# Performance work log

Measured on AMD Instinct MI355X. Metric: run time of the kernel, lower is better.

The kernel has to match this reference:

```python
import jax, jax.numpy as jnp
import numpy as np
import math

NUM_HEADS = 16
SEGMENT_SIZE = 128
DILATION = 2


def hilbert_map(seq_len: int) -> np.ndarray:
    """Boustrophedon ('Hilbert') permutation, matching the torch reference."""
    if seq_len <= 64:
        return np.arange(seq_len, dtype=np.int64)
    g = int(math.ceil(math.sqrt(seq_len)))
    fm = np.zeros(seq_len, dtype=np.int64)
    idx = 0
    for row in range(g):
        cols = range(g) if row % 2 == 0 else range(g - 1, -1, -1)
        for col in cols:
            lp = row * g + col
            if lp < seq_len and idx < seq_len:
                fm[lp] = idx
                idx += 1
    return fm


def setup_inputs() -> dict:
    key = jax.random.key(0)
    k1, k2, k3 = jax.random.split(key, 3)
    B, S, D = 2, 8192, 1024
    x = jax.random.normal(k1, (B, S, D), dtype=jnp.float32)
    W_qkv = jax.random.normal(k2, (D, 3 * D), dtype=jnp.float32) * 0.02
    W_out = jax.random.normal(k3, (D, D), dtype=jnp.float32) * 0.02
    return {"x": x, "W_qkv": W_qkv, "W_out": W_out}


def reference(x, W_qkv, W_out):
    B, S, Dm = x.shape
    H, Dh = NUM_HEADS, Dm // NUM_HEADS
    seg, dil = SEGMENT_SIZE, DILATION
    scale = Dh ** -0.5

    qkv = (x @ W_qkv).reshape(B, S, 3, H, Dh)
    q = jnp.transpose(qkv[:, :, 0], (0, 2, 1, 3))  # [B,H,S,Dh]
    k = jnp.transpose(qkv[:, :, 1], (0, 2, 1, 3))
    v = jnp.transpose(qkv[:, :, 2], (0, 2, 1, 3))

    # Hilbert reorder (active since S > 64)
    m = jnp.asarray(hilbert_map(S))
    q, k, v = q[:, :, m], k[:, :, m], v[:, :, m]

    # Vectorized segment-local dilated attention (S % seg == 0 here)
    nseg = S // seg
    qs = q.reshape(B, H, nseg, seg, Dh)
    ks = k.reshape(B, H, nseg, seg, Dh)[:, :, :, ::dil]  # dilated keys
    vs = v.reshape(B, H, nseg, seg, Dh)[:, :, :, ::dil]
    scores = jnp.einsum('bhnqd,bhnkd->bhnqk', qs, ks) * scale
    attn = jax.nn.softmax(scores, axis=-1)
    out = jnp.einsum('bhnqk,bhnkd->bhnqd', attn, vs).reshape(B, H, S, Dh)

    # Reverse Hilbert ordering
    inv = jnp.argsort(m)
    out = out[:, :, inv]

    out = jnp.transpose(out, (0, 2, 1, 3)).reshape(B, S, Dm)
    return out @ W_out
```

## Files before the change

kernel.cpp:

```cpp
#include <hip/hip_runtime.h>
#include <stdint.h>

typedef unsigned short ushort_t;
typedef __bf16 bf16x8 __attribute__((ext_vector_type(8)));
typedef float  f32x4  __attribute__((ext_vector_type(4)));
typedef float  f32x16 __attribute__((ext_vector_type(16)));

#define DEV static __device__ __forceinline__

DEV ushort_t f2bf(float f){
  union { float f; unsigned u; } x; x.f = f;
  unsigned u = x.u;
  return (ushort_t)((u + 0x7fffu + ((u >> 16) & 1u)) >> 16);
}

DEV int hmap(int p){
  int r = p / 91;
  int c = p - r * 91;
  return (r & 1) ? (r * 91 + 90 - c) : p;
}

DEV void async16(const void* g, void* l){
  __builtin_amdgcn_global_load_lds(
      (const __attribute__((address_space(1))) unsigned*)g,
      (__attribute__((address_space(3))) unsigned*)l, 16, 0, 0);
}

template<int GATHER>
DEV int arow_map(int r){
  if (GATHER == 0) return r;
  if (GATHER == 1){ int b = r >> 13, p = r & 8191; return b * 8192 + hmap(p); }
  int b = r >> 12, rem = r & 4095, seg = rem >> 6, j = rem & 63;
  return b * 8192 + hmap(seg * 128 + 2 * j);
}

__global__ void cast_kernel(const float* __restrict__ in, ushort_t* __restrict__ out, int n4){
  int i = blockIdx.x * blockDim.x + threadIdx.x;
  if (i < n4){
    float4 v = ((const float4*)in)[i];
    ushort4 o;
    o.x = f2bf(v.x); o.y = f2bf(v.y); o.z = f2bf(v.z); o.w = f2bf(v.w);
    ((ushort4*)out)[i] = o;
  }
}

__global__ void transpose_cast(const float* __restrict__ W, ushort_t* __restrict__ WT,
                               int rows, int cols){
  __shared__ ushort_t t[64 * 66];
  int tid = threadIdx.x;
  int c0 = blockIdx.x * 64, r0 = blockIdx.y * 64;
  int cl = tid & 63, rb = tid >> 6;
  for (int i = 0; i < 16; ++i){
    int r = rb + i * 4;
    t[r * 66 + cl] = f2bf(W[(size_t)(r0 + r) * cols + c0 + cl]);
  }
  __syncthreads();
  int rr = tid & 63, cb = tid >> 6;
  for (int i = 0; i < 16; ++i){
    int cc = cb + i * 4;
    WT[(size_t)(c0 + cc) * rows + r0 + rr] = t[rr * 66 + cc];
  }
}

template<int OUT_BF16, int GATHER>
__global__ __launch_bounds__(256, 2) void gemm_bt(const ushort_t* __restrict__ A,
                                                  const ushort_t* __restrict__ BT,
                                                  void* __restrict__ Cout,
                                                  int M, int N, int K){
  __shared__ ushort_t As[128 * 64];
  __shared__ ushort_t Bs[256 * 64];
  int tid  = threadIdx.x;
  int lane = tid & 63, w = tid >> 6;
  int l31 = lane & 31, lh = lane >> 5;

  int mtc = M >> 7;
  int o  = blockIdx.x;
  int nt = o / mtc, mt = o - nt * mtc;
  int m0 = mt * 128, n0 = nt * 256;

  int wm = (w >> 1) * 64, wn = (w & 1) * 128;

  f32x16 acc[2][4];
  #pragma unroll
  for (int a = 0; a < 8; ++a)
    #pragma unroll
    for (int b = 0; b < 16; ++b) acc[a >> 2][a & 3][b] = 0.f;

  int rbase = tid >> 3, slot = tid & 7;
  int g0 = (slot ^ (rbase & 7)) * 8;
  size_t asrc[4];
  #pragma unroll
  for (int i = 0; i < 4; ++i)
    asrc[i] = (size_t)arow_map<GATHER>(m0 + rbase + 32 * i) * K + g0;
  size_t bsrc0 = (size_t)(n0 + rbase) * K + g0;

  int aoff[2][4], boff[4][4];
  #pragma unroll
  for (int mi = 0; mi < 2; ++mi){
    int r = wm + mi * 32 + l31;
    #pragma unroll
    for (int kc = 0; kc < 4; ++kc)
      aoff[mi][kc] = r * 64 + ((kc * 2 + lh) ^ (r & 7)) * 8;
  }
  #pragma unroll
  for (int ni = 0; ni < 4; ++ni){
    int r = wn + ni * 32 + l31;
    #pragma unroll
    for (int kc = 0; kc < 4; ++kc)
      boff[ni][kc] = r * 64 + ((kc * 2 + lh) ^ (r & 7)) * 8;
  }

  for (int k0 = 0; k0 < K; k0 += 64){
    __syncthreads();
    #pragma unroll
    for (int i = 0; i < 4; ++i)
      async16(&A[asrc[i] + k0], &As[(size_t)(256 * i + tid) * 8]);
    #pragma unroll
    for (int i = 0; i < 8; ++i)
      async16(&BT[bsrc0 + (size_t)(32 * i) * K + k0], &Bs[(size_t)(256 * i + tid) * 8]);
    __syncthreads();

    #pragma unroll
    for (int kc = 0; kc < 4; ++kc){
      bf16x8 af[2], bg[4];
      af[0] = *(const bf16x8*)&As[aoff[0][kc]];
      af[1] = *(const bf16x8*)&As[aoff[1][kc]];
      #pragma unroll
      for (int ni = 0; ni < 4; ++ni)
        bg[ni] = *(const bf16x8*)&Bs[boff[ni][kc]];
      #pragma unroll
      for (int mi = 0; mi < 2; ++mi)
        #pragma unroll
        for (int ni = 0; ni < 4; ++ni)
          acc[mi][ni] = __builtin_amdgcn_mfma_f32_32x32x16_bf16(af[mi], bg[ni], acc[mi][ni], 0, 0, 0);
    }
  }

  #pragma unroll
  for (int mi = 0; mi < 2; ++mi){
    #pragma unroll
    for (int ni = 0; ni < 4; ++ni){
      f32x16 v = acc[mi][ni];
      #pragma unroll
      for (int reg = 0; reg < 16; ++reg){
        int r = m0 + wm + mi * 32 + (reg & 3) + 8 * (reg >> 2) + 4 * lh;
        size_t idx = (size_t)r * N + n0 + wn + ni * 32 + l31;
        if (OUT_BF16) ((ushort_t*)Cout)[idx] = f2bf(v[reg]);
        else          ((float*)   Cout)[idx] = v[reg];
      }
    }
  }
}

__global__ __launch_bounds__(256) void attn_kernel(const ushort_t* __restrict__ Qb,
                                                   const ushort_t* __restrict__ KV,
                                                   ushort_t* __restrict__ aout){
  __shared__ ushort_t Qs[128 * 72];
  __shared__ ushort_t Ks[64 * 72];
  __shared__ ushort_t Vt[64 * 72];
  int tid  = threadIdx.x;
  int lane = tid & 63, w = tid >> 6;
  int qd = lane >> 4, md = lane & 15;
  int seg = blockIdx.x, h = blockIdx.y, b = blockIdx.z;
  int p0 = seg * 128;

  for (int it = 0; it < 4; ++it){
    int q = it * 256 + tid;
    int r = q >> 3, ch = q & 7;
    uint4 d = *(const uint4*)&Qb[(size_t)(b * 8192 + p0 + r) * 1024 + h * 64 + ch * 8];
    *(uint4*)&Qs[r * 72 + ch * 8] = d;
  }
  for (int it = 0; it < 2; ++it){
    int q = it * 256 + tid;
    int r = q >> 3, ch = q & 7;
    uint4 d = *(const uint4*)&KV[(size_t)(b * 4096 + seg * 64 + r) * 2048 + h * 64 + ch * 8];
    *(uint4*)&Ks[r * 72 + ch * 8] = d;
  }
  for (int it = 0; it < 2; ++it){
    int q = it * 256 + tid;
    int r = q >> 3, ch = q & 7;
    union { uint4 v; ushort_t u[8]; } d;
    d.v = *(const uint4*)&KV[(size_t)(b * 4096 + seg * 64 + r) * 2048 + 1024 + h * 64 + ch * 8];
    for (int e = 0; e < 8; ++e) Vt[(ch * 8 + e) * 72 + r] = d.u[e];
  }
  __syncthreads();

  f32x4 z = {0.f, 0.f, 0.f, 0.f};
  f32x4 sc[2][4];
  for (int mi = 0; mi < 2; ++mi) for (int ni = 0; ni < 4; ++ni) sc[mi][ni] = z;
  for (int kc = 0; kc < 2; ++kc){
    bf16x8 aq[2], bk[4];
    for (int mi = 0; mi < 2; ++mi)
      aq[mi] = *(const bf16x8*)&Qs[(w * 32 + mi * 16 + md) * 72 + kc * 32 + qd * 8];
    for (int ni = 0; ni < 4; ++ni)
      bk[ni] = *(const bf16x8*)&Ks[(ni * 16 + md) * 72 + kc * 32 + qd * 8];
    for (int mi = 0; mi < 2; ++mi)
      for (int ni = 0; ni < 4; ++ni)
        sc[mi][ni] = __builtin_amdgcn_mfma_f32_16x16x32_bf16(aq[mi], bk[ni], sc[mi][ni], 0, 0, 0);
  }

  const float scale = 0.125f;
  ushort_t* Ps = Qs;
  for (int mi = 0; mi < 2; ++mi){
    for (int i = 0; i < 4; ++i){
      float mx = sc[mi][0][i];
      for (int ni = 1; ni < 4; ++ni) mx = fmaxf(mx, sc[mi][ni][i]);
      for (int d = 1; d < 16; d <<= 1) mx = fmaxf(mx, __shfl_xor(mx, d));
      float e[4], sum = 0.f;
      for (int ni = 0; ni < 4; ++ni){ e[ni] = __expf((sc[mi][ni][i] - mx) * scale); sum += e[ni]; }
      for (int d = 1; d < 16; d <<= 1) sum += __shfl_xor(sum, d);
      float inv = 1.0f / sum;
      int r = w * 32 + mi * 16 + qd * 4 + i;
      for (int ni = 0; ni < 4; ++ni)
        Ps[r * 72 + ni * 16 + md] = f2bf(e[ni] * inv);
    }
  }

  f32x4 oc[2][4];
  for (int mi = 0; mi < 2; ++mi) for (int ni = 0; ni < 4; ++ni) oc[mi][ni] = z;
  for (int kc = 0; kc < 2; ++kc){
    bf16x8 ap[2], bv[4];
    for (int mi = 0; mi < 2; ++mi)
      ap[mi] = *(const bf16x8*)&Ps[(w * 32 + mi * 16 + md) * 72 + kc * 32 + qd * 8];
    for (int ni = 0; ni < 4; ++ni)
      bv[ni] = *(const bf16x8*)&Vt[(ni * 16 + md) * 72 + kc * 32 + qd * 8];
    for (int mi = 0; mi < 2; ++mi)
      for (int ni = 0; ni < 4; ++ni)
        oc[mi][ni] = __builtin_amdgcn_mfma_f32_16x16x32_bf16(ap[mi], bv[ni], oc[mi][ni], 0, 0, 0);
  }

  for (int mi = 0; mi < 2; ++mi){
    for (int i = 0; i < 4; ++i){
      int rl = w * 32 + mi * 16 + qd * 4 + i;
      for (int ni = 0; ni < 4; ++ni)
        Ps[rl * 72 + ni * 16 + md] = f2bf(oc[mi][ni][i]);
    }
  }
  __syncthreads();
  for (int it = 0; it < 4; ++it){
    int q = it * 256 + tid;
    int r = q >> 3, ch = q & 7;
    int s = hmap(p0 + r);
    *(uint4*)&aout[(size_t)(b * 8192 + s) * 1024 + h * 64 + ch * 8] =
        *(const uint4*)&Qs[r * 72 + ch * 8];
  }
}

extern "C" void kernel_launch(void* const* d_in, const int* in_sizes, int n_in,
                              void* d_out, int out_size, void* d_ws, size_t ws_size,
                              hipStream_t stream){
  const float* x    = (const float*)d_in[0];
  const float* Wqkv = (const float*)d_in[1];
  const float* Wout = (const float*)d_in[2];
  float* out = (float*)d_out;

  char* ws = (char*)d_ws;
  ushort_t* xb    = (ushort_t*)(ws);
  ushort_t* WqT   = (ushort_t*)(ws + 33554432);
  ushort_t* WoT   = (ushort_t*)(ws + 39845888);
  ushort_t* Qbuf  = (ushort_t*)(ws + 41943040);
  ushort_t* KVbuf = (ushort_t*)(ws + 75497472);
  ushort_t* aoutb = (ushort_t*)(ws + 109051904);

  cast_kernel<<<16384, 256, 0, stream>>>(x, xb, (16384 * 1024) / 4);
  transpose_cast<<<dim3(48, 16), 256, 0, stream>>>(Wqkv, WqT, 1024, 3072);
  transpose_cast<<<dim3(16, 16), 256, 0, stream>>>(Wout, WoT, 1024, 1024);
  gemm_bt<1, 1><<<4 * 128, 256, 0, stream>>>(xb, WqT, Qbuf, 16384, 1024, 1024);
  gemm_bt<1, 2><<<8 * 64, 256, 0, stream>>>(xb, WqT + (size_t)1024 * 1024, KVbuf, 8192, 2048, 1024);
  attn_kernel<<<dim3(64, 16, 2), 256, 0, stream>>>(Qbuf, KVbuf, aoutb);
  gemm_bt<0, 0><<<4 * 128, 256, 0, stream>>>(aoutb, WoT, out, 16384, 1024, 1024);
}
```

Before: 274.0 us.

## Rewrite GEMM as 256x256 tile, 512-thread, double-buffered async pipeline with XCD swizzle

After: 273.2 us. No clear change (-0.3%).

```diff
diff --git a/kernel.cpp b/kernel.cpp
--- a/kernel.cpp
+++ b/kernel.cpp
@@ -4,7 +4,6 @@
 typedef unsigned short ushort_t;
 typedef __bf16 bf16x8 __attribute__((ext_vector_type(8)));
 typedef float  f32x4  __attribute__((ext_vector_type(4)));
-typedef float  f32x16 __attribute__((ext_vector_type(16)));
 
 #define DEV static __device__ __forceinline__
 
@@ -62,91 +61,124 @@
   }
 }
 
+
+#define BARRIER() asm volatile("s_barrier" ::: "memory")
+#define LGKM0()   asm volatile("s_waitcnt lgkmcnt(0)" ::: "memory")
+#define VMCNT4()  asm volatile("s_waitcnt vmcnt(4)" ::: "memory")
+#define VMCNT0()  asm volatile("s_waitcnt vmcnt(0)" ::: "memory")
+
+#define STAGE_A(T1, HT)                                                        \
+  if ((T1) < NT){                                                              \
+    ushort_t* d_ = &smem[((((T1) & 1)) << 15) + ((HT) << 13) + tid * 8];       \
+    async16(&A[asrc[HT][0] + (size_t)(T1) * 64], d_);                          \
+    async16(&A[asrc[HT][1] + (size_t)(T1) * 64], d_ + 4096);                   \
+  }
+
+#define STAGE_B(T2, HT)                                                        \
+  if ((T2) < NT){                                                              \
+    ushort_t* d_ = &smem[((((T2) & 1)) << 15) + 16384 + ((HT) << 13) + tid * 8];\
+    async16(&BT[bsrc[HT][0] + (size_t)(T2) * 64], d_);                         \
+    async16(&BT[bsrc[HT][1] + (size_t)(T2) * 64], d_ + 4096);                  \
+  }
+
+#define PHASE(MI0, STAGE_STMT, PRE_BAR2)                                       \
+  {                                                                            \
+    bf16x8 af[2][2];                                                           \
+    _Pragma("unroll") for (int m2 = 0; m2 < 2; ++m2)                           \
+      _Pragma("unroll") for (int kk = 0; kk < 2; ++kk)                         \
+        af[m2][kk] = *(const bf16x8*)&Ab[((MI0) + m2) * 1024 + axor[kk]];      \
+    STAGE_STMT;                                                                \
+    BARRIER();                                                                 \
+    LGKM0();                                                                   \
+    __builtin_amdgcn_s_setprio(1);                                             \
+    _Pragma("unroll") for (int kk = 0; kk < 2; ++kk)                           \
+      _Pragma("unroll") for (int ni = 0; ni < 4; ++ni)                         \
+        _Pragma("unroll") for (int m2 = 0; m2 < 2; ++m2)                       \
+          acc[(MI0) + m2][ni] = __builtin_amdgcn_mfma_f32_16x16x32_bf16(       \
+              af[m2][kk], bv[ni][kk], acc[(MI0) + m2][ni], 0, 0, 0);           \
+    __builtin_amdgcn_s_setprio(0);                                             \
+    PRE_BAR2;                                                                  \
+    BARRIER();                                                                 \
+  }
+
 template<int OUT_BF16, int GATHER>
-__global__ __launch_bounds__(256, 2) void gemm_bt(const ushort_t* __restrict__ A,
+__global__ __launch_bounds__(512, 2) void gemm_bt(const ushort_t* __restrict__ A,
                                                   const ushort_t* __restrict__ BT,
                                                   void* __restrict__ Cout,
                                                   int M, int N, int K){
-  __shared__ ushort_t As[128 * 64];
-  __shared__ ushort_t Bs[256 * 64];
-  int tid  = threadIdx.x;
+  __shared__ __align__(16) ushort_t smem[65536];
+  const int NT = K >> 6;
+  int tid = threadIdx.x;
   int lane = tid & 63, w = tid >> 6;
-  int l31 = lane & 31, lh = lane >> 5;
-
-  int mtc = M >> 7;
-  int o  = blockIdx.x;
-  int nt = o / mtc, mt = o - nt * mtc;
-  int m0 = mt * 128, n0 = nt * 256;
-
-  int wm = (w >> 1) * 64, wn = (w & 1) * 128;
-
-  f32x16 acc[2][4];
+  int md = lane & 15, qd = lane >> 4;
+  int wm = w >> 2, wn = w & 3;
+
+  int nwg = gridDim.x;
+  int orig = blockIdx.x;
+  int wg = (orig & 7) * (nwg >> 3) + (orig >> 3);
+  int mtc = M >> 8;
+  int mt = wg % mtc, nt = wg / mtc;
+  int m0 = mt << 8, n0 = nt << 8;
+
+  int rbase = tid >> 3;
+  int g0 = ((tid & 7) ^ (rbase & 7)) * 8;
+  size_t asrc[2][2], bsrc[2][2];
+  #pragma unroll
+  for (int ht = 0; ht < 2; ++ht)
+    #pragma unroll
+    for (int i = 0; i < 2; ++i){
+      asrc[ht][i] = (size_t)arow_map<GATHER>(m0 + ht * 128 + i * 64 + rbase) * K + g0;
+      bsrc[ht][i] = (size_t)(n0 + ht * 128 + i * 64 + rbase) * K + g0;
+    }
+
+  int abase0 = (wm * 128 + md) * 64;
+  int bbase0 = 16384 + (wn * 64 + md) * 64;
+  int axor[2] = { (qd ^ (md & 7)) * 8, ((4 + qd) ^ (md & 7)) * 8 };
+
+  f32x4 acc[8][4];
   #pragma unroll
   for (int a = 0; a < 8; ++a)
     #pragma unroll
-    for (int b = 0; b < 16; ++b) acc[a >> 2][a & 3][b] = 0.f;
-
-  int rbase = tid >> 3, slot = tid & 7;
-  int g0 = (slot ^ (rbase & 7)) * 8;
-  size_t asrc[4];
+    for (int b = 0; b < 4; ++b)
+      #pragma unroll
+      for (int e = 0; e < 4; ++e) acc[a][b][e] = 0.f;
+
+  STAGE_B(0, 0); STAGE_B(0, 1);
+  STAGE_A(0, 0); STAGE_A(0, 1);
+  STAGE_B(1, 0); STAGE_B(1, 1);
+  VMCNT4();
+  BARRIER();
+
+  for (int t = 0; t < NT; ++t){
+    const ushort_t* Ab = &smem[((t & 1) << 15) + abase0];
+    const ushort_t* Bb = &smem[((t & 1) << 15) + bbase0];
+
+    bf16x8 bv[4][2];
+    #pragma unroll
+    for (int ni = 0; ni < 4; ++ni)
+      #pragma unroll
+      for (int kk = 0; kk < 2; ++kk)
+        bv[ni][kk] = *(const bf16x8*)&Bb[ni * 1024 + axor[kk]];
+
+    PHASE(0, STAGE_A(t + 1, 0), ((void)0));
+    PHASE(2, STAGE_A(t + 1, 1), ((void)0));
+    PHASE(4, STAGE_B(t + 2, 0), ((void)0));
+    PHASE(6, STAGE_B(t + 2, 1),
+          if (t < NT - 2) VMCNT4(); else VMCNT0());
+  }
+
+  int crow0 = m0 + wm * 128 + qd * 4;
+  int ccol0 = n0 + wn * 64 + md;
   #pragma unroll
-  for (int i = 0; i < 4; ++i)
-    asrc[i] = (size_t)arow_map<GATHER>(m0 + rbase + 32 * i) * K + g0;
-  size_t bsrc0 = (size_t)(n0 + rbase) * K + g0;
-
-  int aoff[2][4], boff[4][4];
-  #pragma unroll
-  for (int mi = 0; mi < 2; ++mi){
-    int r = wm + mi * 32 + l31;
-    #pragma unroll
-    for (int kc = 0; kc < 4; ++kc)
-      aoff[mi][kc] = r * 64 + ((kc * 2 + lh) ^ (r & 7)) * 8;
-  }
-  #pragma unroll
-  for (int ni = 0; ni < 4; ++ni){
-    int r = wn + ni * 32 + l31;
-    #pragma unroll
-    for (int kc = 0; kc < 4; ++kc)
-      boff[ni][kc] = r * 64 + ((kc * 2 + lh) ^ (r & 7)) * 8;
-  }
-
-  for (int k0 = 0; k0 < K; k0 += 64){
-    __syncthreads();
-    #pragma unroll
-    for (int i = 0; i < 4; ++i)
-      async16(&A[asrc[i] + k0], &As[(size_t)(256 * i + tid) * 8]);
-    #pragma unroll
-    for (int i = 0; i < 8; ++i)
-      async16(&BT[bsrc0 + (size_t)(32 * i) * K + k0], &Bs[(size_t)(256 * i + tid) * 8]);
-    __syncthreads();
-
-    #pragma unroll
-    for (int kc = 0; kc < 4; ++kc){
-      bf16x8 af[2], bg[4];
-      af[0] = *(const bf16x8*)&As[aoff[0][kc]];
-      af[1] = *(const bf16x8*)&As[aoff[1][kc]];
-      #pragma unroll
-      for (int ni = 0; ni < 4; ++ni)
-        bg[ni] = *(const bf16x8*)&Bs[boff[ni][kc]];
-      #pragma unroll
-      for (int mi = 0; mi < 2; ++mi)
-        #pragma unroll
-        for (int ni = 0; ni < 4; ++ni)
-          acc[mi][ni] = __builtin_amdgcn_mfma_f32_32x32x16_bf16(af[mi], bg[ni], acc[mi][ni], 0, 0, 0);
-    }
-  }
-
-  #pragma unroll
-  for (int mi = 0; mi < 2; ++mi){
+  for (int mi = 0; mi < 8; ++mi){
     #pragma unroll
     for (int ni = 0; ni < 4; ++ni){
-      f32x16 v = acc[mi][ni];
+      f32x4 v = acc[mi][ni];
       #pragma unroll
-      for (int reg = 0; reg < 16; ++reg){
-        int r = m0 + wm + mi * 32 + (reg & 3) + 8 * (reg >> 2) + 4 * lh;
-        size_t idx = (size_t)r * N + n0 + wn + ni * 32 + l31;
-        if (OUT_BF16) ((ushort_t*)Cout)[idx] = f2bf(v[reg]);
-        else          ((float*)   Cout)[idx] = v[reg];
+      for (int r = 0; r < 4; ++r){
+        size_t idx = (size_t)(crow0 + mi * 16 + r) * N + ccol0 + ni * 16;
+        if (OUT_BF16) ((ushort_t*)Cout)[idx] = f2bf(v[r]);
+        else          ((float*)   Cout)[idx] = v[r];
       }
     }
   }
@@ -265,8 +297,8 @@
   cast_kernel<<<16384, 256, 0, stream>>>(x, xb, (16384 * 1024) / 4);
   transpose_cast<<<dim3(48, 16), 256, 0, stream>>>(Wqkv, WqT, 1024, 3072);
   transpose_cast<<<dim3(16, 16), 256, 0, stream>>>(Wout, WoT, 1024, 1024);
-  gemm_bt<1, 1><<<4 * 128, 256, 0, stream>>>(xb, WqT, Qbuf, 16384, 1024, 1024);
-  gemm_bt<1, 2><<<8 * 64, 256, 0, stream>>>(xb, WqT + (size_t)1024 * 1024, KVbuf, 8192, 2048, 1024);
+  gemm_bt<1, 1><<<dim3(256), dim3(512), 0, stream>>>(xb, WqT, Qbuf, 16384, 1024, 1024);
+  gemm_bt<1, 2><<<dim3(256), dim3(512), 0, stream>>>(xb, WqT + (size_t)1024 * 1024, KVbuf, 8192, 2048, 1024);
   attn_kernel<<<dim3(64, 16, 2), 256, 0, stream>>>(Qbuf, KVbuf, aoutb);
-  gemm_bt<0, 0><<<4 * 128, 256, 0, stream>>>(aoutb, WoT, out, 16384, 1024, 1024);
-}
+  gemm_bt<0, 0><<<dim3(256), dim3(512), 0, stream>>>(aoutb, WoT, out, 16384, 1024, 1024);
+}
```
